# Kernel optimization log

Measured on AMD Instinct MI355X. Metric: run time of the kernel, lower is better.

Reference implementation:

```python
import jax, jax.numpy as jnp
import numpy as np

SEQ, B, NP, NG = 100, 200, 512, 4096

def setup_inputs() -> dict:
    key = jax.random.key(0)
    ks = jax.random.split(key, 6)
    velocity = jax.random.normal(ks[0], (SEQ, B, 2), dtype=jnp.float32)
    init_pc = jax.random.uniform(ks[1], (B, NP), dtype=jnp.float32)
    # encoder: nn.Linear(Np, Ng, bias=False) -> weight (Ng, Np), default kaiming-uniform-ish; use uniform(+-1/sqrt(Np))
    lim_enc = 1.0 / np.sqrt(NP)
    W_enc = jax.random.uniform(ks[2], (NG, NP), minval=-lim_enc, maxval=lim_enc, dtype=jnp.float32)
    # RNN weights: weight_ih_l0 (Ng, 2), weight_hh_l0 (Ng, Ng); torch init uniform(+-1/sqrt(Ng))
    lim = 1.0 / np.sqrt(NG)
    W_ih = jax.random.uniform(ks[3], (NG, 2), minval=-lim, maxval=lim, dtype=jnp.float32)
    W_hh = jax.random.uniform(ks[4], (NG, NG), minval=-lim, maxval=lim, dtype=jnp.float32)
    # decoder: xavier_uniform on (Np, Ng)
    lim_dec = np.sqrt(6.0 / (NP + NG))
    W_dec = jax.random.uniform(ks[5], (NP, NG), minval=-lim_dec, maxval=lim_dec, dtype=jnp.float32)
    return {"velocity": velocity, "init_pc": init_pc, "W_enc": W_enc,
            "W_ih": W_ih, "W_hh": W_hh, "W_dec": W_dec}

def reference(velocity, init_pc, W_enc, W_ih, W_hh, W_dec):
    # h0 = encoder(init_pc): (B, Ng)
    h0 = init_pc @ W_enc.T
    # precompute input projections for all steps: (SEQ, B, Ng)
    vx = jnp.einsum('sbi,gi->sbg', velocity, W_ih)
    def step(h, v_t):
        h_new = jax.nn.relu(v_t + h @ W_hh.T)
        return h_new, h_new
    _, g = jax.lax.scan(step, h0, vx)          # g: (SEQ, B, Ng)
    place_logits = jnp.einsum('sbg,pg->sbp', g, W_dec)  # (SEQ, B, Np)
    return place_logits, g
```

## Files before the change

### kernel.cpp

```cpp
#include <hip/hip_runtime.h>
#include <cstdint>
#include <cstddef>

#define kSEQ 100
#define kB   200
#define kNP  512
#define kNG  4096
#define kMP  256
#define KSPLIT 8

typedef _Float16 f16_t;
typedef f16_t f16x8 __attribute__((ext_vector_type(8)));
typedef f16_t f16x4 __attribute__((ext_vector_type(4)));
typedef float f32x4 __attribute__((ext_vector_type(4)));

__device__ __forceinline__ void gld_lds16(const f16_t* g, f16_t* l) {
    __builtin_amdgcn_global_load_lds(
        (const __attribute__((address_space(1))) unsigned int*)g,
        (__attribute__((address_space(3))) unsigned int*)l, 16, 0, 0);
}

__global__ __launch_bounds__(256)
void k_half(const float* __restrict__ src, f16_t* __restrict__ dst, int n8) {
    int i = blockIdx.x * 256 + threadIdx.x;
    if (i >= n8) return;
    const float4* s = (const float4*)src + (size_t)i * 2;
    float4 v0 = s[0], v1 = s[1];
    f16x8 h;
    h[0] = (f16_t)v0.x; h[1] = (f16_t)v0.y; h[2] = (f16_t)v0.z; h[3] = (f16_t)v0.w;
    h[4] = (f16_t)v1.x; h[5] = (f16_t)v1.y; h[6] = (f16_t)v1.z; h[7] = (f16_t)v1.w;
    *(f16x8*)(dst + (size_t)i * 8) = h;
}

__global__ __launch_bounds__(512, 4)
void k_gemm_f16(const f16_t* __restrict__ A, int lda,
                const f16_t* __restrict__ B, int ldb,
                f16_t* __restrict__ part, int kPerChunk) {
    __shared__ __align__(16) f16_t sA[2][128 * 64];
    __shared__ __align__(16) f16_t sB[2][128 * 64];

    const int bid    = blockIdx.x;
    const int xcd    = bid & 7;
    const int idx    = bid >> 3;
    const int n_tile = xcd * 4 + (idx & 3);
    const int rem    = idx >> 2;
    const int kc     = rem >> 1;
    const int m_tile = rem & 1;

    const int tid  = threadIdx.x;
    const int lane = tid & 63;
    const int wid  = tid >> 6;
    const int wr   = wid >> 2;
    const int wc   = wid & 3;
    const int m0   = m_tile * 128;
    const int n0   = n_tile * 128;
    const int kBase = kc * kPerChunk;
    const int nIter = kPerChunk >> 6;

    f32x4 acc[4][2];
#pragma unroll
    for (int i = 0; i < 4; i++)
#pragma unroll
        for (int j = 0; j < 2; j++) acc[i][j] = (f32x4){0.f, 0.f, 0.f, 0.f};

    const int s0   = wid * 128 + lane;
    const int s1   = s0 + 64;
    const int r0s  = s0 >> 3, c0 = (s0 & 7) ^ (r0s & 7);
    const int r1s  = s1 >> 3, c1 = (s1 & 7) ^ (r1s & 7);
    const int b0   = (wid * 128) * 8;
    const int b1   = (wid * 128 + 64) * 8;

    const f16_t* gA0 = A + (size_t)(m0 + r0s) * (size_t)lda + c0 * 8;
    const f16_t* gA1 = A + (size_t)(m0 + r1s) * (size_t)lda + c1 * 8;
    const f16_t* gB0 = B + (size_t)(n0 + r0s) * (size_t)ldb + c0 * 8;
    const f16_t* gB1 = B + (size_t)(n0 + r1s) * (size_t)ldb + c1 * 8;

    gld_lds16(gA0 + kBase, &sA[0][b0]);
    gld_lds16(gA1 + kBase, &sA[0][b1]);
    gld_lds16(gB0 + kBase, &sB[0][b0]);
    gld_lds16(gB1 + kBase, &sB[0][b1]);
    __syncthreads();

    int cur = 0;
    for (int kb = 0; kb < nIter; ++kb) {
        if (kb + 1 < nIter) {
            const int kn = kBase + (kb + 1) * 64;
            gld_lds16(gA0 + kn, &sA[cur ^ 1][b0]);
            gld_lds16(gA1 + kn, &sA[cur ^ 1][b1]);
            gld_lds16(gB0 + kn, &sB[cur ^ 1][b0]);
            gld_lds16(gB1 + kn, &sB[cur ^ 1][b1]);
        }
        const f16_t* cA = sA[cur];
        const f16_t* cB = sB[cur];
#pragma unroll
        for (int ks2 = 0; ks2 < 2; ks2++) {
            f16x8 a[4], b[2];
            const unsigned int klane = (unsigned)(lane >> 4) * 16u + (unsigned)ks2 * 64u;
#pragma unroll
            for (int fm = 0; fm < 4; fm++) {
                const unsigned int row = (unsigned)(wr * 64 + fm * 16 + (lane & 15));
                const unsigned int off = (row * 128u + klane) ^ ((row & 7u) << 4);
                a[fm] = *(const f16x8*)((const char*)cA + off);
            }
#pragma unroll
            for (int fn = 0; fn < 2; fn++) {
                const unsigned int row = (unsigned)(wc * 32 + fn * 16 + (lane & 15));
                const unsigned int off = (row * 128u + klane) ^ ((row & 7u) << 4);
                b[fn] = *(const f16x8*)((const char*)cB + off);
            }
#pragma unroll
            for (int fm = 0; fm < 4; fm++)
#pragma unroll
                for (int fn = 0; fn < 2; fn++)
                    acc[fm][fn] = __builtin_amdgcn_mfma_f32_16x16x32_f16(a[fm], b[fn], acc[fm][fn], 0, 0, 0);
        }
        __syncthreads();
        cur ^= 1;
    }

    f16_t* po = part + (size_t)kc * ((size_t)kB * kNG);
#pragma unroll
    for (int fm = 0; fm < 4; fm++)
#pragma unroll
        for (int fn = 0; fn < 2; fn++) {
            const int row0 = m0 + wr * 64 + fm * 16 + ((lane >> 4) << 2);
            const int col  = n0 + wc * 32 + fn * 16 + (lane & 15);
#pragma unroll
            for (int j = 0; j < 4; j++) {
                const int row = row0 + j;
                if (row < kB)
                    po[(size_t)row * kNG + col] = (f16_t)acc[fm][fn][j];
            }
        }
}

__global__ __launch_bounds__(256)
void k_reduce(const f16_t* __restrict__ part,
              const float* __restrict__ velocity, const float* __restrict__ W_ih,
              float* __restrict__ gout, f16_t* __restrict__ gb,
              f16_t* __restrict__ hout, int t, int mode) {
    const int b = blockIdx.y;
    const int g = blockIdx.x * 1024 + threadIdx.x * 4;

    float v0 = 0.f, v1 = 0.f, v2 = 0.f, v3 = 0.f;
#pragma unroll
    for (int ks = 0; ks < KSPLIT; ks++) {
        f16x4 p = *(const f16x4*)(part + (size_t)ks * ((size_t)kB * kNG) + (size_t)b * kNG + g);
        v0 += (float)p[0]; v1 += (float)p[1]; v2 += (float)p[2]; v3 += (float)p[3];
    }
    if (mode == 1) {
        const float2 vel = *(const float2*)(velocity + ((size_t)t * kB + b) * 2);
        const float4 w01 = *(const float4*)(W_ih + (size_t)g * 2);
        const float4 w23 = *(const float4*)(W_ih + (size_t)g * 2 + 4);
        v0 = fmaxf(0.f, v0 + vel.x * w01.x + vel.y * w01.y);
        v1 = fmaxf(0.f, v1 + vel.x * w01.z + vel.y * w01.w);
        v2 = fmaxf(0.f, v2 + vel.x * w23.x + vel.y * w23.y);
        v3 = fmaxf(0.f, v3 + vel.x * w23.z + vel.y * w23.w);
        float4 o; o.x = v0; o.y = v1; o.z = v2; o.w = v3;
        *(float4*)(gout + ((size_t)t * kB + b) * kNG + g) = o;
    }
    f16x4 h;
    h[0] = (f16_t)v0; h[1] = (f16_t)v1; h[2] = (f16_t)v2; h[3] = (f16_t)v3;
    if (hout)
        *(f16x4*)(hout + (size_t)b * kNG + g) = h;
    if (mode == 1 && gb)
        *(f16x4*)(gb + ((size_t)t * kB + b) * kNG + g) = h;
}

__global__ __launch_bounds__(512, 4)
void k_dec_fast(const f16_t* __restrict__ G, const f16_t* __restrict__ Wd,
                float* __restrict__ out) {
    __shared__ __align__(16) f16_t sA[2][128 * 64];
    __shared__ __align__(16) f16_t sB[2][128 * 64];

    const int bid  = blockIdx.x;
    const int xcd  = bid & 7;
    const int idx  = bid >> 3;
    const int tile = xcd * 79 + idx;
    if (tile >= 157 * 4) return;
    const int m0 = (tile >> 2) * 128;
    const int n0 = (tile & 3) * 128;

    const int tid  = threadIdx.x;
    const int lane = tid & 63;
    const int wid  = tid >> 6;
    const int wr   = wid >> 2;
    const int wc   = wid & 3;
    const int M    = kSEQ * kB;

    f32x4 acc[4][2];
#pragma unroll
    for (int i = 0; i < 4; i++)
#pragma unroll
        for (int j = 0; j < 2; j++) acc[i][j] = (f32x4){0.f, 0.f, 0.f, 0.f};

    const int s0   = wid * 128 + lane;
    const int s1   = s0 + 64;
    const int r0s  = s0 >> 3, c0 = (s0 & 7) ^ (r0s & 7);
    const int r1s  = s1 >> 3, c1 = (s1 & 7) ^ (r1s & 7);
    const int b0   = (wid * 128) * 8;
    const int b1   = (wid * 128 + 64) * 8;

    const f16_t* gA0 = G + (size_t)(m0 + r0s) * kNG + c0 * 8;
    const f16_t* gA1 = G + (size_t)(m0 + r1s) * kNG + c1 * 8;
    const f16_t* gB0 = Wd + (size_t)(n0 + r0s) * kNG + c0 * 8;
    const f16_t* gB1 = Wd + (size_t)(n0 + r1s) * kNG + c1 * 8;

    gld_lds16(gA0, &sA[0][b0]);
    gld_lds16(gA1, &sA[0][b1]);
    gld_lds16(gB0, &sB[0][b0]);
    gld_lds16(gB1, &sB[0][b1]);
    __syncthreads();

    int cur = 0;
    for (int kb = 0; kb < kNG / 64; ++kb) {
        if (kb + 1 < kNG / 64) {
            const int kn = (kb + 1) * 64;
            gld_lds16(gA0 + kn, &sA[cur ^ 1][b0]);
            gld_lds16(gA1 + kn, &sA[cur ^ 1][b1]);
            gld_lds16(gB0 + kn, &sB[cur ^ 1][b0]);
            gld_lds16(gB1 + kn, &sB[cur ^ 1][b1]);
        }
        const f16_t* cA = sA[cur];
        const f16_t* cB = sB[cur];
#pragma unroll
        for (int ks2 = 0; ks2 < 2; ks2++) {
            f16x8 a[4], b[2];
            const unsigned int klane = (unsigned)(lane >> 4) * 16u + (unsigned)ks2 * 64u;
#pragma unroll
            for (int fm = 0; fm < 4; fm++) {
                const unsigned int row = (unsigned)(wr * 64 + fm * 16 + (lane & 15));
                const unsigned int off = (row * 128u + klane) ^ ((row & 7u) << 4);
                a[fm] = *(const f16x8*)((const char*)cA + off);
            }
#pragma unroll
            for (int fn = 0; fn < 2; fn++) {
                const unsigned int row = (unsigned)(wc * 32 + fn * 16 + (lane & 15));
                const unsigned int off = (row * 128u + klane) ^ ((row & 7u) << 4);
                b[fn] = *(const f16x8*)((const char*)cB + off);
            }
#pragma unroll
            for (int fm = 0; fm < 4; fm++)
#pragma unroll
                for (int fn = 0; fn < 2; fn++)
                    acc[fm][fn] = __builtin_amdgcn_mfma_f32_16x16x32_f16(a[fm], b[fn], acc[fm][fn], 0, 0, 0);
        }
        __syncthreads();
        cur ^= 1;
    }

#pragma unroll
    for (int fm = 0; fm < 4; fm++)
#pragma unroll
        for (int fn = 0; fn < 2; fn++) {
            const int row0 = m0 + wr * 64 + fm * 16 + ((lane >> 4) << 2);
            const int col  = n0 + wc * 32 + fn * 16 + (lane & 15);
#pragma unroll
            for (int j = 0; j < 4; j++) {
                const int row = row0 + j;
                if (row < M) out[(size_t)row * kNP + col] = acc[fm][fn][j];
            }
        }
}

__global__ __launch_bounds__(256)
void k_dec(const float* __restrict__ Gf, const f16_t* __restrict__ Wd,
           float* __restrict__ out) {
    __shared__ __align__(16) f16_t sA[128 * 64];
    __shared__ __align__(16) f16_t sB[128 * 64];

    const int bid  = blockIdx.x;
    const int xcd  = bid & 7;
    const int idx  = bid >> 3;
    const int tile = xcd * 79 + idx;
    if (tile >= 157 * 4) return;
    const int m0 = (tile >> 2) * 128;
    const int n0 = (tile & 3) * 128;

    const int tid  = threadIdx.x;
    const int lane = tid & 63;
    const int wid  = tid >> 6;
    const int wr   = wid >> 1;
    const int wc   = wid & 1;
    const int M    = kSEQ * kB;

    f32x4 acc[4][4];
#pragma unroll
    for (int i = 0; i < 4; i++)
#pragma unroll
        for (int j = 0; j < 4; j++) acc[i][j] = (f32x4){0.f, 0.f, 0.f, 0.f};

    const int sr   = tid >> 1;
    const int half = tid & 1;
    const int sc   = half * 32;
    const unsigned int swzrow = ((unsigned)sr & 7u) << 4;
    const unsigned int sbase  = (unsigned)sr * 128u + (unsigned)half * 64u;
    int arow = m0 + sr; if (arow > M - 1) arow = M - 1;

    for (int k0 = 0; k0 < kNG; k0 += 64) {
        __syncthreads();
        {
            const float4* gA = (const float4*)(Gf + (size_t)arow * kNG + k0 + sc);
#pragma unroll
            for (int i = 0; i < 4; i++) {
                float4 a0 = gA[2 * i], a1 = gA[2 * i + 1];
                f16x8 u;
                u[0] = (f16_t)a0.x; u[1] = (f16_t)a0.y; u[2] = (f16_t)a0.z; u[3] = (f16_t)a0.w;
                u[4] = (f16_t)a1.x; u[5] = (f16_t)a1.y; u[6] = (f16_t)a1.z; u[7] = (f16_t)a1.w;
                unsigned int off = (sbase + (unsigned)i * 16u) ^ swzrow;
                *(f16x8*)((char*)sA + off) = u;
            }
            const uint4* gB = (const uint4*)(Wd + (size_t)(n0 + sr) * kNG + k0 + sc);
#pragma unroll
            for (int i = 0; i < 4; i++) {
                unsigned int off = (sbase + (unsigned)i * 16u) ^ swzrow;
                *(uint4*)((char*)sB + off) = gB[i];
            }
        }
        __syncthreads();
#pragma unroll
        for (int ks2 = 0; ks2 < 2; ks2++) {
            f16x8 a[4], b[4];
            const unsigned int klane = (unsigned)(lane >> 4) * 16u + (unsigned)ks2 * 64u;
#pragma unroll
            for (int fm = 0; fm < 4; fm++) {
                const unsigned int row = (unsigned)(wr * 64 + fm * 16 + (lane & 15));
                const unsigned int off = (row * 128u + klane) ^ ((row & 7u) << 4);
                a[fm] = *(const f16x8*)((const char*)sA + off);
            }
#pragma unroll
            for (int fn = 0; fn < 4; fn++) {
                const unsigned int row = (unsigned)(wc * 64 + fn * 16 + (lane & 15));
                const unsigned int off = (row * 128u + klane) ^ ((row & 7u) << 4);
                b[fn] = *(const f16x8*)((const char*)sB + off);
            }
#pragma unroll
            for (int fm = 0; fm < 4; fm++)
#pragma unroll
                for (int fn = 0; fn < 4; fn++)
                    acc[fm][fn] = __builtin_amdgcn_mfma_f32_16x16x32_f16(a[fm], b[fn], acc[fm][fn], 0, 0, 0);
        }
    }

#pragma unroll
    for (int fm = 0; fm < 4; fm++)
#pragma unroll
        for (int fn = 0; fn < 4; fn++) {
            const int row0 = m0 + wr * 64 + fm * 16 + ((lane >> 4) << 2);
            const int col  = n0 + wc * 64 + fn * 16 + (lane & 15);
#pragma unroll
            for (int j = 0; j < 4; j++) {
                const int row = row0 + j;
                if (row < M) out[(size_t)row * kNP + col] = acc[fm][fn][j];
            }
        }
}

extern "C" void kernel_launch(void* const* d_in, const int* in_sizes, int n_in,
                              void* d_out, int out_size, void* d_ws, size_t ws_size,
                              hipStream_t stream) {
    const float* velocity = (const float*)d_in[0];
    const float* init_pc  = (const float*)d_in[1];
    const float* W_enc    = (const float*)d_in[2];
    const float* W_ih     = (const float*)d_in[3];
    const float* W_hh     = (const float*)d_in[4];
    const float* W_dec    = (const float*)d_in[5];

    float* logits = (float*)d_out;
    float* gout   = logits + (size_t)kSEQ * kB * kNP;

    char* ws = (char*)d_ws;
    size_t off = 0;
    auto alloc = [&](size_t bytes) -> void* {
        void* p = ws + off;
        off += (bytes + 255) & ~(size_t)255;
        return p;
    };
    f16_t* whh  = (f16_t*)alloc((size_t)kNG * kNG * 2);
    f16_t* wdec = (f16_t*)alloc((size_t)kNP * kNG * 2);
    f16_t* wenc = (f16_t*)alloc((size_t)kNG * kNP * 2);
    f16_t* ip   = (f16_t*)alloc((size_t)kMP * kNP * 2);
    f16_t* h_buf[2];
    h_buf[0] = (f16_t*)alloc((size_t)kMP * kNG * 2);
    h_buf[1] = (f16_t*)alloc((size_t)kMP * kNG * 2);
    f16_t* partial = (f16_t*)alloc((size_t)KSPLIT * kB * kNG * 2);
    f16_t* gb = nullptr;
    if (ws_size >= off + ((size_t)kSEQ * kB + kMP) * kNG * 2 + 4096)
        gb = (f16_t*)alloc(((size_t)kSEQ * kB + kMP) * kNG * 2);

    hipMemsetAsync(ip + (size_t)kB * kNP, 0, (size_t)(kMP - kB) * kNP * 2, stream);

    int n8;
    n8 = kNG * kNG / 8;
    k_half<<<(n8 + 255) / 256, 256, 0, stream>>>(W_hh, whh, n8);
    n8 = kNP * kNG / 8;
    k_half<<<(n8 + 255) / 256, 256, 0, stream>>>(W_dec, wdec, n8);
    n8 = kNG * kNP / 8;
    k_half<<<(n8 + 255) / 256, 256, 0, stream>>>(W_enc, wenc, n8);
    n8 = kB * kNP / 8;
    k_half<<<(n8 + 255) / 256, 256, 0, stream>>>(init_pc, ip, n8);

    dim3 gR(4, kB);

    k_gemm_f16<<<512, 512, 0, stream>>>(ip, kNP, wenc, kNP, partial, kNP / KSPLIT);
    k_reduce<<<gR, 256, 0, stream>>>(partial, velocity, W_ih, nullptr, nullptr, h_buf[0], 0, 0);

    if (gb) {
        const f16_t* Acur = h_buf[0];
        for (int t = 0; t < kSEQ; t++) {
            k_gemm_f16<<<512, 512, 0, stream>>>(Acur, kNG, whh, kNG, partial, kNG / KSPLIT);
            k_reduce<<<gR, 256, 0, stream>>>(partial, velocity, W_ih, gout, gb, nullptr, t, 1);
            Acur = gb + (size_t)t * kB * kNG;
        }
    } else {
        int p = 0;
        for (int t = 0; t < kSEQ; t++) {
            k_gemm_f16<<<512, 512, 0, stream>>>(h_buf[p], kNG, whh, kNG, partial, kNG / KSPLIT);
            k_reduce<<<gR, 256, 0, stream>>>(partial, velocity, W_ih, gout, nullptr, h_buf[p ^ 1], t, 1);
            p ^= 1;
        }
    }

    if (gb)
        k_dec_fast<<<632, 512, 0, stream>>>(gb, wdec, logits);
    else
        k_dec<<<632, 256, 0, stream>>>(gout, wdec, logits);
}
```

Measured before the change: 2.114 ms.

## Use wider-N GEMM tiles with 16-way K split and XCD-aware tile mapping for scan

Adds a scan-step GEMM that uses 128x256 output tiles, each wave covering 64x64, with a 16-way K split. Block IDs are mapped so that each XCD owns a contiguous pair of N tiles, which should keep its slice of W_hh resident in that XCD's L2 across timesteps. The reduce kernel now takes the split count at runtime. In exchange, each block does less K work and writes twice as many fp16 partials, so the reduce pass reads more data.

```diff
diff --git a/kernel.cpp b/kernel.cpp
--- a/kernel.cpp
+++ b/kernel.cpp
@@ -7,7 +7,8 @@
 #define kNP  512
 #define kNG  4096
 #define kMP  256
-#define KSPLIT 8
+#define KSP_ENC 8
+#define KSP_SCAN 16
 
 typedef _Float16 f16_t;
 typedef f16_t f16x8 __attribute__((ext_vector_type(8)));
@@ -134,8 +135,116 @@
         }
 }
 
+__global__ __launch_bounds__(512, 4)
+void k_gemm_wide(const f16_t* __restrict__ A,
+                 const f16_t* __restrict__ B,
+                 f16_t* __restrict__ part) {
+    __shared__ __align__(16) f16_t sA[128 * 64];
+    __shared__ __align__(16) f16_t sB[256 * 64];
+
+    const int bid    = blockIdx.x;
+    const int xcd    = bid & 7;
+    const int idx    = bid >> 3;
+    const int n_tile = xcd * 2 + (idx & 1);
+    const int rem    = idx >> 1;
+    const int kc     = rem >> 1;
+    const int m_tile = rem & 1;
+
+    const int tid  = threadIdx.x;
+    const int lane = tid & 63;
+    const int wid  = tid >> 6;
+    const int wr   = wid >> 2;
+    const int wc   = wid & 3;
+    const int m0   = m_tile * 128;
+    const int n0   = n_tile * 256;
+    const int kPer = kNG / KSP_SCAN;
+    const int kBase = kc * kPer;
+    const int nIter = kPer >> 6;
+
+    f32x4 acc[4][4];
+#pragma unroll
+    for (int i = 0; i < 4; i++)
+#pragma unroll
+        for (int j = 0; j < 4; j++) acc[i][j] = (f32x4){0.f, 0.f, 0.f, 0.f};
+
+    const int sa0 = wid * 128 + lane;
+    const int sa1 = sa0 + 64;
+    const int ra0 = sa0 >> 3, ca0 = (sa0 & 7) ^ (ra0 & 7);
+    const int ra1 = sa1 >> 3, ca1 = (sa1 & 7) ^ (ra1 & 7);
+    const int sb0 = wid * 256 + lane;
+    const int rb0 = sb0 >> 3,        cb0 = (sb0 & 7) ^ (rb0 & 7);
+    const int rb1 = (sb0 + 64) >> 3, cb1 = ((sb0 + 64) & 7) ^ (rb1 & 7);
+    const int rb2 = (sb0 + 128) >> 3, cb2 = ((sb0 + 128) & 7) ^ (rb2 & 7);
+    const int rb3 = (sb0 + 192) >> 3, cb3 = ((sb0 + 192) & 7) ^ (rb3 & 7);
+
+    const f16_t* gA0 = A + (size_t)(m0 + ra0) * kNG + ca0 * 8 + kBase;
+    const f16_t* gA1 = A + (size_t)(m0 + ra1) * kNG + ca1 * 8 + kBase;
+    const f16_t* gB0 = B + (size_t)(n0 + rb0) * kNG + cb0 * 8 + kBase;
+    const f16_t* gB1 = B + (size_t)(n0 + rb1) * kNG + cb1 * 8 + kBase;
+    const f16_t* gB2 = B + (size_t)(n0 + rb2) * kNG + cb2 * 8 + kBase;
+    const f16_t* gB3 = B + (size_t)(n0 + rb3) * kNG + cb3 * 8 + kBase;
+    f16_t* dA0 = sA + (size_t)sa0 * 8 - (size_t)lane * 8;
+    f16_t* dA1 = sA + (size_t)(sa0 + 64) * 8 - (size_t)lane * 8;
+    f16_t* dB0 = sB + (size_t)sb0 * 8 - (size_t)lane * 8;
+    f16_t* dB1 = sB + (size_t)(sb0 + 64) * 8 - (size_t)lane * 8;
+    f16_t* dB2 = sB + (size_t)(sb0 + 128) * 8 - (size_t)lane * 8;
+    f16_t* dB3 = sB + (size_t)(sb0 + 192) * 8 - (size_t)lane * 8;
+    dA0 += (size_t)lane * 8; dA1 += (size_t)lane * 8;
+    dB0 += (size_t)lane * 8; dB1 += (size_t)lane * 8;
+    dB2 += (size_t)lane * 8; dB3 += (size_t)lane * 8;
+
+    for (int kb = 0; kb < nIter; ++kb) {
+        const int k0 = kb * 64;
+        __syncthreads();
+        gld_lds16(gA0 + k0, dA0);
+        gld_lds16(gA1 + k0, dA1);
+        gld_lds16(gB0 + k0, dB0);
+        gld_lds16(gB1 + k0, dB1);
+        gld_lds16(gB2 + k0, dB2);
+        gld_lds16(gB3 + k0, dB3);
+        __syncthreads();
+#pragma unroll
+        for (int ks2 = 0; ks2 < 2; ks2++) {
+            f16x8 a[4], b[4];
+            const unsigned int klane = (unsigned)(lane >> 4) * 16u + (unsigned)ks2 * 64u;
+#pragma unroll
+            for (int fm = 0; fm < 4; fm++) {
+                const unsigned int row = (unsigned)(wr * 64 + fm * 16 + (lane & 15));
+                const unsigned int off = (row * 128u + klane) ^ ((row & 7u) << 4);
+                a[fm] = *(const f16x8*)((const char*)sA + off);
+            }
+#pragma unroll
+            for (int fn = 0; fn < 4; fn++) {
+                const unsigned int row = (unsigned)(wc * 64 + fn * 16 + (lane & 15));
+                const unsigned int off = (row * 128u + klane) ^ ((row & 7u) << 4);
+                b[fn] = *(const f16x8*)((const char*)sB + off);
+            }
+#pragma unroll
+            for (int fm = 0; fm < 4; fm++)
+#pragma unroll
+                for (int fn = 0; fn < 4; fn++)
+                    acc[fm][fn] = __builtin_amdgcn_mfma_f32_16x16x32_f16(a[fm], b[fn], acc[fm][fn], 0, 0, 0);
+        }
+    }
+
+    f16_t* po = part + (size_t)kc * ((size_t)kB * kNG);
+#pragma unroll
+    for (int fm = 0; fm < 4; fm++)
+#pragma unroll
+        for (int fn = 0; fn < 4; fn++) {
+            const int row0 = m0 + wr * 64 + fm * 16 + ((lane >> 4) << 2);
+            const int col  = n0 + wc * 64 + fn * 16 + (lane & 15);
+#pragma unroll
+            for (int j = 0; j < 4; j++) {
+                const int row = row0 + j;
+                if (row < kB)
+                    po[(size_t)row * kNG + col] = (f16_t)acc[fm][fn][j];
+            }
+        }
+}
+
 __global__ __launch_bounds__(256)
-void k_reduce(const f16_t* __restrict__ part,
+void k_reduce(const f16_t* __restrict__ part, int nsplit,
               const float* __restrict__ velocity, const float* __restrict__ W_ih,
               float* __restrict__ gout, f16_t* __restrict__ gb,
               f16_t* __restrict__ hout, int t, int mode) {
@@ -143,8 +252,7 @@
     const int g = blockIdx.x * 1024 + threadIdx.x * 4;
 
     float v0 = 0.f, v1 = 0.f, v2 = 0.f, v3 = 0.f;
-#pragma unroll
-    for (int ks = 0; ks < KSPLIT; ks++) {
+    for (int ks = 0; ks < nsplit; ks++) {
         f16x4 p = *(const f16x4*)(part + (size_t)ks * ((size_t)kB * kNG) + (size_t)b * kNG + g);
         v0 += (float)p[0]; v1 += (float)p[1]; v2 += (float)p[2]; v3 += (float)p[3];
     }
@@ -383,7 +491,7 @@
     f16_t* h_buf[2];
     h_buf[0] = (f16_t*)alloc((size_t)kMP * kNG * 2);
     h_buf[1] = (f16_t*)alloc((size_t)kMP * kNG * 2);
-    f16_t* partial = (f16_t*)alloc((size_t)KSPLIT * kB * kNG * 2);
+    f16_t* partial = (f16_t*)alloc((size_t)KSP_SCAN * kB * kNG * 2);
     f16_t* gb = nullptr;
     if (ws_size >= off + ((size_t)kSEQ * kB + kMP) * kNG * 2 + 4096)
         gb = (f16_t*)alloc(((size_t)kSEQ * kB + kMP) * kNG * 2);
@@ -402,21 +510,21 @@
 
     dim3 gR(4, kB);
 
-    k_gemm_f16<<<512, 512, 0, stream>>>(ip, kNP, wenc, kNP, partial, kNP / KSPLIT);
-    k_reduce<<<gR, 256, 0, stream>>>(partial, velocity, W_ih, nullptr, nullptr, h_buf[0], 0, 0);
+    k_gemm_f16<<<512, 512, 0, stream>>>(ip, kNP, wenc, kNP, partial, kNP / KSP_ENC);
+    k_reduce<<<gR, 256, 0, stream>>>(partial, KSP_ENC, velocity, W_ih, nullptr, nullptr, h_buf[0], 0, 0);
 
     if (gb) {
         const f16_t* Acur = h_buf[0];
         for (int t = 0; t < kSEQ; t++) {
-            k_gemm_f16<<<512, 512, 0, stream>>>(Acur, kNG, whh, kNG, partial, kNG / KSPLIT);
-            k_reduce<<<gR, 256, 0, stream>>>(partial, velocity, W_ih, gout, gb, nullptr, t, 1);
+            k_gemm_wide<<<512, 512, 0, stream>>>(Acur, whh, partial);
+            k_reduce<<<gR, 256, 0, stream>>>(partial, KSP_SCAN, velocity, W_ih, gout, gb, nullptr, t, 1);
             Acur = gb + (size_t)t * kB * kNG;
         }
     } else {
         int p = 0;
         for (int t = 0; t < kSEQ; t++) {
-            k_gemm_f16<<<512, 512, 0, stream>>>(h_buf[p], kNG, whh, kNG, partial, kNG / KSPLIT);
-            k_reduce<<<gR, 256, 0, stream>>>(partial, velocity, W_ih, gout, nullptr, h_buf[p ^ 1], t, 1);
+            k_gemm_wide<<<512, 512, 0, stream>>>(h_buf[p], whh, partial);
+            k_reduce<<<gR, 256, 0, stream>>>(partial, KSP_SCAN, velocity, W_ih, gout, nullptr, h_buf[p ^ 1], t, 1);
             p ^= 1;
         }
     }
```

After: 2.592 ms. 22.6% more time.
